# Performance work log

Hardware: AMD Instinct MI355X
Metric: run time of the kernel (lower is better)

## Reference

```python
import jax, jax.numpy as jnp
import numpy as np
import math

D_MODEL, N_HEAD, N_KV_HEAD, MAX_LEN = 2048, 32, 8, 2048
D_K = D_MODEL // N_HEAD
BASE = 10000.0
B, T = 2, 2048


def _rope_tables(seq_len):
    # matches torch Rotary: cos/sin of shape [seq_len, D_K], repeat_interleave(2) over freq dim
    inv_freq = 1.0 / (BASE ** (jnp.arange(0, D_K, 2, dtype=jnp.float32) / D_K))
    t = jnp.arange(seq_len, dtype=jnp.float32)[:, None] * inv_freq  # [T, D_K/2]
    cos = jnp.repeat(jnp.cos(t), 2, axis=-1)  # [T, D_K]
    sin = jnp.repeat(jnp.sin(t), 2, axis=-1)
    return cos, sin


def _rotate_half(x):
    # faithful to source: x1 = even lanes, x2 = odd lanes, concat([-x2, x1], -1)
    x1, x2 = x[..., ::2], x[..., 1::2]
    return jnp.concatenate([-x2, x1], axis=-1)


def _apply_rope(x, cos, sin):
    return x * cos + _rotate_half(x) * sin


def setup_inputs() -> dict:
    key = jax.random.key(0)
    ks = jax.random.split(key, 5)
    s = 1.0 / math.sqrt(D_MODEL)
    x = jax.random.normal(ks[0], (B, T, D_MODEL), dtype=jnp.float32)
    Wq = jax.random.normal(ks[1], (D_MODEL, N_HEAD * D_K), dtype=jnp.float32) * s
    Wk = jax.random.normal(ks[2], (D_MODEL, N_KV_HEAD * D_K), dtype=jnp.float32) * s
    Wv = jax.random.normal(ks[3], (D_MODEL, N_KV_HEAD * D_K), dtype=jnp.float32) * s
    Wo = jax.random.normal(ks[4], (N_HEAD * D_K, D_MODEL), dtype=jnp.float32) * s
    mask = jnp.tril(jnp.ones((T, T), dtype=bool))  # causal
    return {"x": x, "mask": mask, "Wq": Wq, "Wk": Wk, "Wv": Wv, "Wo": Wo}


def reference(x, mask, Wq, Wk, Wv, Wo):
    b, t, _ = x.shape
    g = N_HEAD // N_KV_HEAD
    q = (x @ Wq).reshape(b, t, N_HEAD, D_K).transpose(0, 2, 1, 3)      # [B,H,T,d]
    k = (x @ Wk).reshape(b, t, N_KV_HEAD, D_K).transpose(0, 2, 1, 3)   # [B,Hkv,T,d]
    v = (x @ Wv).reshape(b, t, N_KV_HEAD, D_K).transpose(0, 2, 1, 3)
    cos, sin = _rope_tables(t)
    q = _apply_rope(q, cos, sin)
    k = _apply_rope(k, cos, sin)  # rope before/after repeat is identical per-head
    # grouped attention: q head h attends kv head h // g (repeat_interleave semantics)
    qg = q.reshape(b, N_KV_HEAD, g, t, D_K)
    scores = jnp.einsum("bkgtd,bksd->bkgts", qg, k) / math.sqrt(D_K)
    neg = jnp.finfo(scores.dtype).min
    scores = jnp.where(mask[None, None, None, :, :], scores, neg)
    attn = jax.nn.softmax(scores, axis=-1)
    out = jnp.einsum("bkgts,bksd->bkgtd", attn, v)
    out = out.reshape(b, N_HEAD, t, D_K).transpose(0, 2, 1, 3).reshape(b, t, N_HEAD * D_K)
    return out @ Wo
```

## Files before the change

### kernel.cpp

```cpp
#include <hip/hip_runtime.h>
#include <cstdint>
#include <cstddef>

typedef unsigned short u16;
typedef __attribute__((ext_vector_type(8))) short bf16x8;
typedef __attribute__((ext_vector_type(8))) unsigned short u16x8;
typedef __attribute__((ext_vector_type(4))) unsigned short u16x4;
typedef __attribute__((ext_vector_type(4))) float f32x4;

__device__ __forceinline__ unsigned short f2bf(float f) {
    union { float f; uint32_t u; } c; c.f = f;
    uint32_t u = c.u + 0x7fffu + ((c.u >> 16) & 1u);
    return (unsigned short)(u >> 16);
}
__device__ __forceinline__ float bf2f(unsigned short h) {
    union { uint32_t u; float f; } c; c.u = ((uint32_t)h) << 16;
    return c.f;
}
__device__ __forceinline__ uint32_t cvtpk(float a, float b) {
    uint32_t r;
    asm("v_cvt_pk_bf16_f32 %0, %1, %2" : "=v"(r) : "v"(a), "v"(b));
    return r;
}

#define GLDS16(g, l)                                                               \
    __builtin_amdgcn_global_load_lds((const __attribute__((address_space(1))) void*)(g), \
                                     (__attribute__((address_space(3))) void*)(l), 16, 0, 0)

__global__ __launch_bounds__(256) void cvt_x(const float* __restrict__ src,
                                             u16* __restrict__ dst) {
    int i = blockIdx.x * 256 + threadIdx.x;
    const float4* s = (const float4*)src + (size_t)i * 2;
    float4 a = s[0], b = s[1];
    u16x8 o;
    o[0] = f2bf(a.x); o[1] = f2bf(a.y); o[2] = f2bf(a.z); o[3] = f2bf(a.w);
    o[4] = f2bf(b.x); o[5] = f2bf(b.y); o[6] = f2bf(b.z); o[7] = f2bf(b.w);
    *(u16x8*)(dst + (size_t)i * 8) = o;
}

__global__ __launch_bounds__(256) void tcvt(const float* __restrict__ src,
                                            u16* __restrict__ dst, int C) {
    __shared__ u16 tile[32][33];
    const int t = threadIdx.x;
    const int bx = blockIdx.x, by = blockIdx.y;
    const int tr = t >> 3, tc = (t & 7) << 2;
    float4 f = *(const float4*)&src[(size_t)(by * 32 + tr) * C + bx * 32 + tc];
    tile[tr][tc + 0] = f2bf(f.x); tile[tr][tc + 1] = f2bf(f.y);
    tile[tr][tc + 2] = f2bf(f.z); tile[tr][tc + 3] = f2bf(f.w);
    __syncthreads();
    u16x4 o;
    o[0] = tile[tc + 0][tr]; o[1] = tile[tc + 1][tr];
    o[2] = tile[tc + 2][tr]; o[3] = tile[tc + 3][tr];
    *(u16x4*)&dst[(size_t)(bx * 32 + tr) * 2048 + by * 32 + tc] = o;
}

__global__ __launch_bounds__(256) void tcvt3(const float* __restrict__ Wq,
                                             const float* __restrict__ Wk,
                                             const float* __restrict__ Wv,
                                             u16* __restrict__ dst) {
    __shared__ u16 tile[32][33];
    const int t = threadIdx.x;
    const int bxg = blockIdx.x, by = blockIdx.y;
    const float* src; int C, nb; u16* dbase;
    if (bxg < 64)      { src = Wq; C = 2048; nb = bxg;      dbase = dst; }
    else if (bxg < 80) { src = Wk; C = 512;  nb = bxg - 64; dbase = dst + (size_t)2048 * 2048; }
    else               { src = Wv; C = 512;  nb = bxg - 80; dbase = dst + (size_t)2560 * 2048; }
    const int tr = t >> 3, tc = (t & 7) << 2;
    float4 f = *(const float4*)&src[(size_t)(by * 32 + tr) * C + nb * 32 + tc];
    tile[tr][tc + 0] = f2bf(f.x); tile[tr][tc + 1] = f2bf(f.y);
    tile[tr][tc + 2] = f2bf(f.z); tile[tr][tc + 3] = f2bf(f.w);
    __syncthreads();
    u16x4 o;
    o[0] = tile[tc + 0][tr]; o[1] = tile[tc + 1][tr];
    o[2] = tile[tc + 2][tr]; o[3] = tile[tc + 3][tr];
    *(u16x4*)&dbase[(size_t)(nb * 32 + tr) * 2048 + by * 32 + tc] = o;
}

template <int MODE>
__global__ __launch_bounds__(256) void gemm2(const u16* __restrict__ A,
                                             const u16* __restrict__ Bt,
                                             u16* __restrict__ oq, u16* __restrict__ ok,
                                             u16* __restrict__ ov, float* __restrict__ of) {
    __shared__ u16 As[128 * 32];
    __shared__ u16 Bs[128 * 32];
    const int t = threadIdx.x, w = t >> 6, lane = t & 63;
    const int l15 = lane & 15, quad = lane >> 4;
    const int m0 = blockIdx.y << 7, n0 = blockIdx.x << 7;
    const int K = 2048;
    const int c0 = w * 2, c1 = c0 + 1;
    const int ar0 = c0 * 16 + (lane >> 2), ar1 = c1 * 16 + (lane >> 2);
    const int ac = (lane & 3) << 3;
    const u16* Ap0 = A + (size_t)(m0 + ar0) * K + ac;
    const u16* Ap1 = A + (size_t)(m0 + ar1) * K + ac;
    const u16* Bp0 = Bt + (size_t)(n0 + ar0) * K + ac;
    const u16* Bp1 = Bt + (size_t)(n0 + ar1) * K + ac;
    const int wm = (w >> 1) << 6, wn = (w & 1) << 6;

    f32x4 acc[4][4] = {};

    for (int k0 = 0; k0 < K; k0 += 32) {
        GLDS16(Ap0 + k0, &As[c0 * 512]);
        GLDS16(Ap1 + k0, &As[c1 * 512]);
        GLDS16(Bp0 + k0, &Bs[c0 * 512]);
        GLDS16(Bp1 + k0, &Bs[c1 * 512]);
        __syncthreads();
        bf16x8 a[4], bfr[4];
#pragma unroll
        for (int mt = 0; mt < 4; ++mt)
            a[mt] = *(bf16x8*)&As[(wm + mt * 16 + l15) * 32 + quad * 8];
#pragma unroll
        for (int nt = 0; nt < 4; ++nt)
            bfr[nt] = *(bf16x8*)&Bs[(wn + nt * 16 + l15) * 32 + quad * 8];
#pragma unroll
        for (int mt = 0; mt < 4; ++mt)
#pragma unroll
            for (int nt = 0; nt < 4; ++nt)
                acc[mt][nt] = __builtin_amdgcn_mfma_f32_16x16x32_bf16(a[mt], bfr[nt], acc[mt][nt], 0, 0, 0);
        __syncthreads();
    }

    if constexpr (MODE == 0) {
        const int colbase = n0 + wn;
        const bool isv = (colbase >= 2560);
        float iv[4];
        if (!isv) {
#pragma unroll
            for (int nt = 0; nt < 4; ++nt)
                iv[nt] = exp2f(-0.4152410118609253f * (float)(nt * 8 + (l15 >> 1)));
        }
        const int map1 = (quad << 4) | ((2 * l15 + 1) & 15);
        const int map2 = (quad << 4) | ((2 * l15) & 15);
        const bool lo = (l15 < 8);
#pragma unroll
        for (int mt = 0; mt < 4; ++mt)
#pragma unroll
            for (int r = 0; r < 4; ++r) {
                const int row = m0 + wm + mt * 16 + quad * 4 + r;
                float v0 = acc[mt][0][r], v1 = acc[mt][1][r];
                float v2 = acc[mt][2][r], v3 = acc[mt][3][r];
                float o0 = v0, o1 = v1, o2 = v2, o3 = v3;
                if (!isv) {
                    float g1a = __shfl(v0, map1), g1b = __shfl(v1, map1);
                    float g1c = __shfl(v2, map1), g1d = __shfl(v3, map1);
                    float g2a = __shfl(v0, map2), g2b = __shfl(v1, map2);
                    float g2c = __shfl(v2, map2), g2d = __shfl(v3, map2);
                    float p0 = lo ? g1a : g1b;
                    float p1 = lo ? g1c : g1d;
                    float p2 = lo ? g2a : g2b;
                    float p3 = lo ? g2c : g2d;
                    const float tt = (float)(row & 2047);
                    float sn, cs;
                    __sincosf(tt * iv[0], &sn, &cs); o0 = v0 * cs - p0 * sn;
                    __sincosf(tt * iv[1], &sn, &cs); o1 = v1 * cs - p1 * sn;
                    __sincosf(tt * iv[2], &sn, &cs); o2 = v2 * cs + p2 * sn;
                    __sincosf(tt * iv[3], &sn, &cs); o3 = v3 * cs + p3 * sn;
                }
                float o[4] = {o0, o1, o2, o3};
                if (colbase < 2048) {
#pragma unroll
                    for (int nt = 0; nt < 4; ++nt)
                        oq[(size_t)row * 2048 + colbase + nt * 16 + l15] = f2bf(o[nt]);
                } else if (colbase < 2560) {
#pragma unroll
                    for (int nt = 0; nt < 4; ++nt)
                        ok[(size_t)row * 512 + colbase - 2048 + nt * 16 + l15] = f2bf(o[nt]);
                } else {
#pragma unroll
                    for (int nt = 0; nt < 4; ++nt)
                        ov[(size_t)(colbase - 2560 + nt * 16 + l15) * 4096 + row] = f2bf(o[nt]);
                }
            }
    } else {
#pragma unroll
        for (int mt = 0; mt < 4; ++mt)
#pragma unroll
            for (int nt = 0; nt < 4; ++nt)
#pragma unroll
                for (int r = 0; r < 4; ++r) {
                    int row = m0 + wm + mt * 16 + quad * 4 + r;
                    int col = n0 + wn + nt * 16 + l15;
                    of[(size_t)row * 2048 + col] = acc[mt][nt][r];
                }
    }
}

__global__ __launch_bounds__(256, 2) void attn8(const u16* __restrict__ q,
                                                const u16* __restrict__ k,
                                                const u16* __restrict__ vT,
                                                u16* __restrict__ att) {
    __shared__ u16 Ks[64 * 64];
    __shared__ u16 Vt[64 * 64];
    __shared__ u16 Pw[4][2][16 * 64];

    const int t = threadIdx.x, w = t >> 6, lane = t & 63;
    const int l15 = lane & 15, quad = lane >> 4;
    const int id = blockIdx.x;
    const int kvh = id & 7;
    const int z = (id >> 3) & 1;
    const int gi = id >> 4;
    const int p = gi & 15;
    int g;
    switch (gi >> 4) {
        case 0:  g = 63 - p; break;
        case 1:  g = 32 + p; break;
        case 2:  g = 31 - p; break;
        default: g = p;      break;
    }
    const int h = kvh * 4 + w;
    const size_t rowbase = (size_t)z * 2048;
    const float SC = 0.125f * 1.4426950408889634f;
    const int swz = l15 & 7;

    const int srow = t >> 3;
    const int slot = t & 7;
    const int sd = slot << 3;
    const int lidx = srow * 64 + ((slot ^ (srow & 7)) << 3);

    const u16* kbase = &k[(rowbase + srow) * 512 + kvh * 64 + sd];
    const u16* vbase = &vT[(size_t)(kvh * 64 + srow) * 4096 + rowbase + sd];

    const int ntiles = (g >> 1) + 1;
    const int qrow0 = g * 32;

    bf16x8 aq[2][2];
#pragma unroll
    for (int m = 0; m < 2; ++m)
#pragma unroll
        for (int kc = 0; kc < 2; ++kc)
            aq[m][kc] = *(const bf16x8*)&q[(rowbase + qrow0 + m * 16 + l15) * 2048 +
                                           h * 64 + kc * 32 + quad * 8];

    f32x4 acc[2][4] = {};
    float m_i[2] = {-INFINITY, -INFINITY};
    float l_i[2] = {0.f, 0.f};

    u16x8 pk0 = *(const u16x8*)kbase;
    u16x8 pk1 = *(const u16x8*)(kbase + (size_t)32 * 512);
    u16x8 pv0 = *(const u16x8*)vbase;
    u16x8 pv1 = *(const u16x8*)(vbase + (size_t)32 * 4096);

    for (int kb = 0; kb < ntiles; ++kb) {
        __syncthreads();
        *(u16x8*)&Ks[lidx]        = pk0;
        *(u16x8*)&Ks[lidx + 2048] = pk1;
        *(u16x8*)&Vt[lidx]        = pv0;
        *(u16x8*)&Vt[lidx + 2048] = pv1;
        if (kb + 1 < ntiles) {
            const u16* kp = kbase + (size_t)(kb + 1) * 64 * 512;
            pk0 = *(const u16x8*)kp;
            pk1 = *(const u16x8*)(kp + (size_t)32 * 512);
            const u16* vp = vbase + (size_t)(kb + 1) * 64;
            pv0 = *(const u16x8*)vp;
            pv1 = *(const u16x8*)(vp + (size_t)32 * 4096);
        }
        __syncthreads();

        f32x4 st[2][4] = {};
        __builtin_amdgcn_s_setprio(1);
#pragma unroll
        for (int kt = 0; kt < 4; ++kt) {
            bf16x8 ak0 = *(const bf16x8*)&Ks[(kt * 16 + l15) * 64 + ((quad ^ swz) << 3)];
            bf16x8 ak1 = *(const bf16x8*)&Ks[(kt * 16 + l15) * 64 + (((quad + 4) ^ swz) << 3)];
#pragma unroll
            for (int m = 0; m < 2; ++m) {
                st[m][kt] = __builtin_amdgcn_mfma_f32_16x16x32_bf16(ak0, aq[m][0], st[m][kt], 0, 0, 0);
                st[m][kt] = __builtin_amdgcn_mfma_f32_16x16x32_bf16(ak1, aq[m][1], st[m][kt], 0, 0, 0);
            }
        }
        __builtin_amdgcn_s_setprio(0);

        const bool diag = (kb == ntiles - 1);
        float alpha_[2];
        bool resc[2];
#pragma unroll
        for (int m = 0; m < 2; ++m) {
            float sv[16];
#pragma unroll
            for (int kt = 0; kt < 4; ++kt)
#pragma unroll
                for (int r = 0; r < 4; ++r) sv[kt * 4 + r] = st[m][kt][r];
            if (diag) {
                const int qg = qrow0 + m * 16 + l15;
#pragma unroll
                for (int kt = 0; kt < 4; ++kt)
#pragma unroll
                    for (int r = 0; r < 4; ++r) {
                        int key = kb * 64 + kt * 16 + quad * 4 + r;
                        if (key > qg) sv[kt * 4 + r] = -INFINITY;
                    }
            }
            float mx = sv[0];
#pragma unroll
            for (int i = 1; i < 16; ++i) mx = fmaxf(mx, sv[i]);
            mx = fmaxf(mx, __shfl_xor(mx, 16));
            mx = fmaxf(mx, __shfl_xor(mx, 32));
            mx *= SC;
            const float mold = m_i[m];
            const bool need = __any(mx > mold + 8.f);
            float al = 1.f;
            if (need) {
                const float mnew = fmaxf(mold, mx);
                al = __builtin_amdgcn_exp2f(mold - mnew);
                m_i[m] = mnew;
            }
            const float mu = m_i[m];
            float sum = 0.f;
#pragma unroll
            for (int i = 0; i < 16; ++i) {
                sv[i] = __builtin_amdgcn_exp2f(fmaf(sv[i], SC, -mu));
                sum += sv[i];
            }
            sum += __shfl_xor(sum, 16);
            sum += __shfl_xor(sum, 32);
            l_i[m] = l_i[m] * al + sum;
            alpha_[m] = al;
            resc[m] = need;

            u16* Pq = &Pw[w][m][0];
#pragma unroll
            for (int kt = 0; kt < 4; ++kt) {
                uint2 uu;
                uu.x = cvtpk(sv[kt * 4 + 0], sv[kt * 4 + 1]);
                uu.y = cvtpk(sv[kt * 4 + 2], sv[kt * 4 + 3]);
                *(uint2*)&Pq[l15 * 64 + (((2 * kt + (quad >> 1)) ^ swz) << 3) + ((quad & 1) << 2)] = uu;
            }
        }

#pragma unroll
        for (int m = 0; m < 2; ++m)
            if (resc[m]) {
                const float al = alpha_[m];
#pragma unroll
                for (int dt = 0; dt < 4; ++dt)
#pragma unroll
                    for (int r = 0; r < 4; ++r) acc[m][dt][r] *= al;
            }

        bf16x8 bp[2][2];
#pragma unroll
        for (int m = 0; m < 2; ++m) {
            const u16* Pq = &Pw[w][m][0];
            bp[m][0] = *(const bf16x8*)&Pq[l15 * 64 + ((quad ^ swz) << 3)];
            bp[m][1] = *(const bf16x8*)&Pq[l15 * 64 + (((quad + 4) ^ swz) << 3)];
        }

        __builtin_amdgcn_s_setprio(1);
#pragma unroll
        for (int dt = 0; dt < 4; ++dt) {
            bf16x8 av0 = *(const bf16x8*)&Vt[(dt * 16 + l15) * 64 + ((quad ^ swz) << 3)];
            bf16x8 av1 = *(const bf16x8*)&Vt[(dt * 16 + l15) * 64 + (((quad + 4) ^ swz) << 3)];
#pragma unroll
            for (int m = 0; m < 2; ++m) {
                acc[m][dt] = __builtin_amdgcn_mfma_f32_16x16x32_bf16(av0, bp[m][0], acc[m][dt], 0, 0, 0);
                acc[m][dt] = __builtin_amdgcn_mfma_f32_16x16x32_bf16(av1, bp[m][1], acc[m][dt], 0, 0, 0);
            }
        }
        __builtin_amdgcn_s_setprio(0);
    }

#pragma unroll
    for (int m = 0; m < 2; ++m) {
        float inv = 1.0f / l_i[m];
        size_t row = rowbase + qrow0 + m * 16 + l15;
#pragma unroll
        for (int dt = 0; dt < 4; ++dt) {
            uint2 uu;
            uu.x = cvtpk(acc[m][dt][0] * inv, acc[m][dt][1] * inv);
            uu.y = cvtpk(acc[m][dt][2] * inv, acc[m][dt][3] * inv);
            *(uint2*)&att[row * 2048 + h * 64 + dt * 16 + quad * 4] = uu;
        }
    }
}

extern "C" void kernel_launch(void* const* d_in, const int* in_sizes, int n_in,
                              void* d_out, int out_size, void* d_ws, size_t ws_size,
                              hipStream_t stream) {
    const float* x  = (const float*)d_in[0];
    const float* Wq = (const float*)d_in[2];
    const float* Wk = (const float*)d_in[3];
    const float* Wv = (const float*)d_in[4];
    const float* Wo = (const float*)d_in[5];
    float* out = (float*)d_out;

    u16* xb = (u16*)d_out;

    u16* q     = (u16*)d_ws;
    u16* kk    = q + (size_t)4096 * 2048;
    u16* vt    = kk + (size_t)4096 * 512;
    u16* wqkvt = vt + (size_t)4096 * 512;
    u16* att   = wqkvt;
    u16* wot   = kk;

    cvt_x<<<4096, 256, 0, stream>>>(x, xb);
    tcvt3<<<dim3(96, 64), 256, 0, stream>>>(Wq, Wk, Wv, wqkvt);
    gemm2<0><<<dim3(24, 32), 256, 0, stream>>>(xb, wqkvt, q, kk, vt, nullptr);
    attn8<<<1024, 256, 0, stream>>>(q, kk, vt, att);
    tcvt<<<dim3(64, 64), 256, 0, stream>>>(Wo, wot, 2048);
    gemm2<1><<<dim3(16, 32), 256, 0, stream>>>(att, wot, nullptr, nullptr, nullptr, out);
}
```

Before: 311.6 us.

## Replace QKV projection GEMM with 256x256 tile, 8-wave ping-pong pipelined kernel

```diff
diff --git a/kernel.cpp b/kernel.cpp
--- a/kernel.cpp
+++ b/kernel.cpp
@@ -119,69 +119,183 @@
         __syncthreads();
     }
 
-    if constexpr (MODE == 0) {
-        const int colbase = n0 + wn;
-        const bool isv = (colbase >= 2560);
-        float iv[4];
-        if (!isv) {
-#pragma unroll
-            for (int nt = 0; nt < 4; ++nt)
-                iv[nt] = exp2f(-0.4152410118609253f * (float)(nt * 8 + (l15 >> 1)));
-        }
-        const int map1 = (quad << 4) | ((2 * l15 + 1) & 15);
-        const int map2 = (quad << 4) | ((2 * l15) & 15);
-        const bool lo = (l15 < 8);
-#pragma unroll
-        for (int mt = 0; mt < 4; ++mt)
+#pragma unroll
+    for (int mt = 0; mt < 4; ++mt)
+#pragma unroll
+        for (int nt = 0; nt < 4; ++nt)
 #pragma unroll
             for (int r = 0; r < 4; ++r) {
-                const int row = m0 + wm + mt * 16 + quad * 4 + r;
-                float v0 = acc[mt][0][r], v1 = acc[mt][1][r];
-                float v2 = acc[mt][2][r], v3 = acc[mt][3][r];
-                float o0 = v0, o1 = v1, o2 = v2, o3 = v3;
-                if (!isv) {
-                    float g1a = __shfl(v0, map1), g1b = __shfl(v1, map1);
-                    float g1c = __shfl(v2, map1), g1d = __shfl(v3, map1);
-                    float g2a = __shfl(v0, map2), g2b = __shfl(v1, map2);
-                    float g2c = __shfl(v2, map2), g2d = __shfl(v3, map2);
-                    float p0 = lo ? g1a : g1b;
-                    float p1 = lo ? g1c : g1d;
-                    float p2 = lo ? g2a : g2b;
-                    float p3 = lo ? g2c : g2d;
-                    const float tt = (float)(row & 2047);
-                    float sn, cs;
-                    __sincosf(tt * iv[0], &sn, &cs); o0 = v0 * cs - p0 * sn;
-                    __sincosf(tt * iv[1], &sn, &cs); o1 = v1 * cs - p1 * sn;
-                    __sincosf(tt * iv[2], &sn, &cs); o2 = v2 * cs + p2 * sn;
-                    __sincosf(tt * iv[3], &sn, &cs); o3 = v3 * cs + p3 * sn;
-                }
-                float o[4] = {o0, o1, o2, o3};
-                if (colbase < 2048) {
-#pragma unroll
-                    for (int nt = 0; nt < 4; ++nt)
-                        oq[(size_t)row * 2048 + colbase + nt * 16 + l15] = f2bf(o[nt]);
-                } else if (colbase < 2560) {
-#pragma unroll
-                    for (int nt = 0; nt < 4; ++nt)
-                        ok[(size_t)row * 512 + colbase - 2048 + nt * 16 + l15] = f2bf(o[nt]);
-                } else {
-#pragma unroll
-                    for (int nt = 0; nt < 4; ++nt)
-                        ov[(size_t)(colbase - 2560 + nt * 16 + l15) * 4096 + row] = f2bf(o[nt]);
-                }
-            }
-    } else {
-#pragma unroll
-        for (int mt = 0; mt < 4; ++mt)
-#pragma unroll
-            for (int nt = 0; nt < 4; ++nt)
-#pragma unroll
-                for (int r = 0; r < 4; ++r) {
-                    int row = m0 + wm + mt * 16 + quad * 4 + r;
-                    int col = n0 + wn + nt * 16 + l15;
-                    of[(size_t)row * 2048 + col] = acc[mt][nt][r];
-                }
-    }
+                int row = m0 + wm + mt * 16 + quad * 4 + r;
+                int col = n0 + wn + nt * 16 + l15;
+                of[(size_t)row * 2048 + col] = acc[mt][nt][r];
+            }
+}
+
+__global__ __launch_bounds__(512, 1) void gemm8p(const u16* __restrict__ A,
+                                                 const u16* __restrict__ Bt,
+                                                 u16* __restrict__ oq, u16* __restrict__ ok,
+                                                 u16* __restrict__ ov) {
+    __shared__ u16 lds[65536];
+
+    const int t = threadIdx.x, w = t >> 6, lane = t & 63;
+    const int l15 = lane & 15, quad = lane >> 4;
+    const int wm = w >> 2, wn = w & 3;
+    const int m0 = blockIdx.y << 8, n0 = blockIdx.x << 8;
+    const int K = 2048;
+    const int NIT = 16;
+
+    const int srow = w * 8 + (lane >> 3);
+    const int scol = ((lane & 7) ^ (lane >> 3)) << 3;
+    const u16* pA = A + (size_t)(m0 + srow) * K + scol;
+    const u16* pB = Bt + (size_t)(n0 + srow) * K + scol;
+
+#define STG(AB, BUF, HF, T) do {                                                   \
+    const u16* _s = ((AB) ? pB : pA) + (size_t)((HF) * 128) * K + (size_t)(T) * 64; \
+    u16* _d = &lds[(BUF) * 32768 + (AB) * 16384 + (HF) * 8192 + w * 512];          \
+    GLDS16(_s, _d);                                                                \
+    GLDS16(_s + (size_t)64 * K, _d + 4096);                                        \
+} while (0)
+
+#define RD_A(BUF, MQ)                                                              \
+    _Pragma("unroll") for (int fi = 0; fi < 4; ++fi)                               \
+    _Pragma("unroll") for (int ks = 0; ks < 2; ++ks) {                             \
+        int r_ = (MQ) * 64 + fi * 16 + l15;                                        \
+        int u_ = ks * 4 + quad;                                                    \
+        a_[fi][ks] = *(const bf16x8*)&lds[(BUF) * 32768 + wm * 8192 + r_ * 64 +    \
+                                          ((u_ ^ (r_ & 7)) << 3)];                 \
+    }
+#define RD_B(BUF, NQ)                                                              \
+    _Pragma("unroll") for (int fj = 0; fj < 2; ++fj)                               \
+    _Pragma("unroll") for (int ks = 0; ks < 2; ++ks) {                             \
+        int r_ = (wn & 1) * 64 + (NQ) * 32 + fj * 16 + l15;                        \
+        int u_ = ks * 4 + quad;                                                    \
+        b_[fj][ks] = *(const bf16x8*)&lds[(BUF) * 32768 + 16384 + (wn >> 1) * 8192 \
+                                          + r_ * 64 + ((u_ ^ (r_ & 7)) << 3)];     \
+    }
+#define MFMA16(MQ, NQ)                                                             \
+    __builtin_amdgcn_s_barrier();                                                  \
+    asm volatile("s_waitcnt lgkmcnt(0)" ::: "memory");                             \
+    __builtin_amdgcn_sched_barrier(0);                                             \
+    __builtin_amdgcn_s_setprio(1);                                                 \
+    _Pragma("unroll") for (int fi = 0; fi < 4; ++fi)                               \
+    _Pragma("unroll") for (int fj = 0; fj < 2; ++fj) {                             \
+        acc[(MQ) * 4 + fi][(NQ) * 2 + fj] = __builtin_amdgcn_mfma_f32_16x16x32_bf16( \
+            a_[fi][0], b_[fj][0], acc[(MQ) * 4 + fi][(NQ) * 2 + fj], 0, 0, 0);     \
+        acc[(MQ) * 4 + fi][(NQ) * 2 + fj] = __builtin_amdgcn_mfma_f32_16x16x32_bf16( \
+            a_[fi][1], b_[fj][1], acc[(MQ) * 4 + fi][(NQ) * 2 + fj], 0, 0, 0);     \
+    }                                                                              \
+    __builtin_amdgcn_s_setprio(0);
+
+    f32x4 acc[8][4] = {};
+    bf16x8 a_[4][2], b_[2][2];
+
+    STG(0, 0, 0, 0); STG(0, 0, 1, 0);
+    STG(1, 0, 0, 0); STG(1, 0, 1, 0);
+    STG(1, 1, 0, 1); STG(1, 1, 1, 1);
+    asm volatile("s_waitcnt vmcnt(4)" ::: "memory");
+    __builtin_amdgcn_s_barrier();
+
+    for (int it = 0; it < NIT; ++it) {
+        const bool more = (it + 1 < NIT);
+        const int o = 2 * it + 1, e2 = 2 * it + 2, o2 = 2 * it + 3;
+
+        RD_A(0, 0); RD_B(0, 0);
+        STG(0, 1, 0, o);
+        MFMA16(0, 0);
+        __builtin_amdgcn_s_barrier();
+
+        RD_A(0, 1);
+        STG(0, 1, 1, o);
+        MFMA16(1, 0);
+        __builtin_amdgcn_s_barrier();
+
+        RD_A(0, 0); RD_B(0, 1);
+        MFMA16(0, 1);
+        __builtin_amdgcn_s_barrier();
+
+        RD_A(0, 1);
+        if (more) { STG(1, 0, 0, e2); STG(1, 0, 1, e2); }
+        MFMA16(1, 1);
+        if (more) asm volatile("s_waitcnt vmcnt(4)" ::: "memory");
+        else      asm volatile("s_waitcnt vmcnt(0)" ::: "memory");
+        __builtin_amdgcn_s_barrier();
+
+        RD_A(1, 0); RD_B(1, 0);
+        if (more) STG(0, 0, 0, e2);
+        MFMA16(0, 0);
+        __builtin_amdgcn_s_barrier();
+
+        RD_A(1, 1);
+        if (more) STG(0, 0, 1, e2);
+        MFMA16(1, 0);
+        __builtin_amdgcn_s_barrier();
+
+        RD_A(1, 0); RD_B(1, 1);
+        MFMA16(0, 1);
+        __builtin_amdgcn_s_barrier();
+
+        RD_A(1, 1);
+        if (more) { STG(1, 1, 0, o2); STG(1, 1, 1, o2); }
+        MFMA16(1, 1);
+        if (more) asm volatile("s_waitcnt vmcnt(4)" ::: "memory");
+        else      asm volatile("s_waitcnt vmcnt(0)" ::: "memory");
+        __builtin_amdgcn_s_barrier();
+    }
+#undef STG
+#undef RD_A
+#undef RD_B
+#undef MFMA16
+
+    const int colbase = n0 + wn * 64;
+    const bool isv = (colbase >= 2560);
+    float iv[4];
+    if (!isv) {
+#pragma unroll
+        for (int nj = 0; nj < 4; ++nj)
+            iv[nj] = exp2f(-0.4152410118609253f * (float)(nj * 8 + (l15 >> 1)));
+    }
+    const int map1 = (quad << 4) | ((2 * l15 + 1) & 15);
+    const int map2 = (quad << 4) | ((2 * l15) & 15);
+    const bool lo = (l15 < 8);
+#pragma unroll
+    for (int mi = 0; mi < 8; ++mi)
+#pragma unroll
+        for (int r = 0; r < 4; ++r) {
+            const int row = m0 + wm * 128 + mi * 16 + quad * 4 + r;
+            float v0 = acc[mi][0][r], v1 = acc[mi][1][r];
+            float v2 = acc[mi][2][r], v3 = acc[mi][3][r];
+            float o0 = v0, o1 = v1, o2 = v2, o3 = v3;
+            if (!isv) {
+                float g1a = __shfl(v0, map1), g1b = __shfl(v1, map1);
+                float g1c = __shfl(v2, map1), g1d = __shfl(v3, map1);
+                float g2a = __shfl(v0, map2), g2b = __shfl(v1, map2);
+                float g2c = __shfl(v2, map2), g2d = __shfl(v3, map2);
+                float p0 = lo ? g1a : g1b;
+                float p1 = lo ? g1c : g1d;
+                float p2 = lo ? g2a : g2b;
+                float p3 = lo ? g2c : g2d;
+                const float tt = (float)(row & 2047);
+                float sn, cs;
+                __sincosf(tt * iv[0], &sn, &cs); o0 = v0 * cs - p0 * sn;
+                __sincosf(tt * iv[1], &sn, &cs); o1 = v1 * cs - p1 * sn;
+                __sincosf(tt * iv[2], &sn, &cs); o2 = v2 * cs + p2 * sn;
+                __sincosf(tt * iv[3], &sn, &cs); o3 = v3 * cs + p3 * sn;
+            }
+            float oo[4] = {o0, o1, o2, o3};
+            if (colbase < 2048) {
+#pragma unroll
+                for (int nj = 0; nj < 4; ++nj)
+                    oq[(size_t)row * 2048 + colbase + nj * 16 + l15] = f2bf(oo[nj]);
+            } else if (colbase < 2560) {
+#pragma unroll
+                for (int nj = 0; nj < 4; ++nj)
+                    ok[(size_t)row * 512 + colbase - 2048 + nj * 16 + l15] = f2bf(oo[nj]);
+            } else {
+#pragma unroll
+                for (int nj = 0; nj < 4; ++nj)
+                    ov[(size_t)(colbase - 2560 + nj * 16 + l15) * 4096 + row] = f2bf(oo[nj]);
+            }
+        }
 }
 
 __global__ __launch_bounds__(256, 2) void attn8(const u16* __restrict__ q,
@@ -393,7 +507,7 @@
 
     cvt_x<<<4096, 256, 0, stream>>>(x, xb);
     tcvt3<<<dim3(96, 64), 256, 0, stream>>>(Wq, Wk, Wv, wqkvt);
-    gemm2<0><<<dim3(24, 32), 256, 0, stream>>>(xb, wqkvt, q, kk, vt, nullptr);
+    gemm8p<<<dim3(12, 16), 512, 0, stream>>>(xb, wqkvt, q, kk, vt);
     attn8<<<1024, 256, 0, stream>>>(q, kk, vt, att);
     tcvt<<<dim3(64, 64), 256, 0, stream>>>(Wo, wot, 2048);
     gemm2<1><<<dim3(16, 32), 256, 0, stream>>>(att, wot, nullptr, nullptr, nullptr, out);
```

Result: slower. 330.7 us (+6.1%).

## Double-buffer K/V tiles in attention and fuse all conversion kernels into one launch

Applied to the files above, without the earlier changes.

```diff
diff --git a/kernel.cpp b/kernel.cpp
--- a/kernel.cpp
+++ b/kernel.cpp
@@ -27,15 +27,49 @@
     __builtin_amdgcn_global_load_lds((const __attribute__((address_space(1))) void*)(g), \
                                      (__attribute__((address_space(3))) void*)(l), 16, 0, 0)
 
-__global__ __launch_bounds__(256) void cvt_x(const float* __restrict__ src,
-                                             u16* __restrict__ dst) {
-    int i = blockIdx.x * 256 + threadIdx.x;
-    const float4* s = (const float4*)src + (size_t)i * 2;
-    float4 a = s[0], b = s[1];
-    u16x8 o;
-    o[0] = f2bf(a.x); o[1] = f2bf(a.y); o[2] = f2bf(a.z); o[3] = f2bf(a.w);
-    o[4] = f2bf(b.x); o[5] = f2bf(b.y); o[6] = f2bf(b.z); o[7] = f2bf(b.w);
-    *(u16x8*)(dst + (size_t)i * 8) = o;
+__global__ __launch_bounds__(256) void prep(const float* __restrict__ x,
+                                            const float* __restrict__ Wq,
+                                            const float* __restrict__ Wk,
+                                            const float* __restrict__ Wv,
+                                            const float* __restrict__ Wo,
+                                            u16* __restrict__ xb,
+                                            u16* __restrict__ wqkvt,
+                                            u16* __restrict__ wot) {
+    __shared__ u16 tile[32][33];
+    const int id = blockIdx.x;
+    const int t = threadIdx.x;
+
+    if (id < 4096) {
+        int i = id * 256 + t;
+        const float4* s = (const float4*)x + (size_t)i * 2;
+        float4 a = s[0], b = s[1];
+        u16x8 o;
+        o[0] = f2bf(a.x); o[1] = f2bf(a.y); o[2] = f2bf(a.z); o[3] = f2bf(a.w);
+        o[4] = f2bf(b.x); o[5] = f2bf(b.y); o[6] = f2bf(b.z); o[7] = f2bf(b.w);
+        *(u16x8*)(xb + (size_t)i * 8) = o;
+        return;
+    }
+
+    const float* src; int C, nb, by; u16* dbase;
+    if (id < 10240) {
+        int r = id - 4096;
+        int bxg = r % 96; by = r / 96;
+        if (bxg < 64)      { src = Wq; C = 2048; nb = bxg;      dbase = wqkvt; }
+        else if (bxg < 80) { src = Wk; C = 512;  nb = bxg - 64; dbase = wqkvt + (size_t)2048 * 2048; }
+        else               { src = Wv; C = 512;  nb = bxg - 80; dbase = wqkvt + (size_t)2560 * 2048; }
+    } else {
+        int r = id - 10240;
+        nb = r % 64; by = r / 64; src = Wo; C = 2048; dbase = wot;
+    }
+    const int tr = t >> 3, tc = (t & 7) << 2;
+    float4 f = *(const float4*)&src[(size_t)(by * 32 + tr) * C + nb * 32 + tc];
+    tile[tr][tc + 0] = f2bf(f.x); tile[tr][tc + 1] = f2bf(f.y);
+    tile[tr][tc + 2] = f2bf(f.z); tile[tr][tc + 3] = f2bf(f.w);
+    __syncthreads();
+    u16x4 o;
+    o[0] = tile[tc + 0][tr]; o[1] = tile[tc + 1][tr];
+    o[2] = tile[tc + 2][tr]; o[3] = tile[tc + 3][tr];
+    *(u16x4*)&dbase[(size_t)(nb * 32 + tr) * 2048 + by * 32 + tc] = o;
 }
 
 __global__ __launch_bounds__(256) void tcvt(const float* __restrict__ src,
@@ -52,28 +86,6 @@
     o[0] = tile[tc + 0][tr]; o[1] = tile[tc + 1][tr];
     o[2] = tile[tc + 2][tr]; o[3] = tile[tc + 3][tr];
     *(u16x4*)&dst[(size_t)(bx * 32 + tr) * 2048 + by * 32 + tc] = o;
-}
-
-__global__ __launch_bounds__(256) void tcvt3(const float* __restrict__ Wq,
-                                             const float* __restrict__ Wk,
-                                             const float* __restrict__ Wv,
-                                             u16* __restrict__ dst) {
-    __shared__ u16 tile[32][33];
-    const int t = threadIdx.x;
-    const int bxg = blockIdx.x, by = blockIdx.y;
-    const float* src; int C, nb; u16* dbase;
-    if (bxg < 64)      { src = Wq; C = 2048; nb = bxg;      dbase = dst; }
-    else if (bxg < 80) { src = Wk; C = 512;  nb = bxg - 64; dbase = dst + (size_t)2048 * 2048; }
-    else               { src = Wv; C = 512;  nb = bxg - 80; dbase = dst + (size_t)2560 * 2048; }
-    const int tr = t >> 3, tc = (t & 7) << 2;
-    float4 f = *(const float4*)&src[(size_t)(by * 32 + tr) * C + nb * 32 + tc];
-    tile[tr][tc + 0] = f2bf(f.x); tile[tr][tc + 1] = f2bf(f.y);
-    tile[tr][tc + 2] = f2bf(f.z); tile[tr][tc + 3] = f2bf(f.w);
-    __syncthreads();
-    u16x4 o;
-    o[0] = tile[tc + 0][tr]; o[1] = tile[tc + 1][tr];
-    o[2] = tile[tc + 2][tr]; o[3] = tile[tc + 3][tr];
-    *(u16x4*)&dbase[(size_t)(nb * 32 + tr) * 2048 + by * 32 + tc] = o;
 }
 
 template <int MODE>
@@ -184,12 +196,12 @@
     }
 }
 
-__global__ __launch_bounds__(256, 2) void attn8(const u16* __restrict__ q,
-                                                const u16* __restrict__ k,
-                                                const u16* __restrict__ vT,
-                                                u16* __restrict__ att) {
-    __shared__ u16 Ks[64 * 64];
-    __shared__ u16 Vt[64 * 64];
+__global__ __launch_bounds__(256, 2) void attn10(const u16* __restrict__ q,
+                                                 const u16* __restrict__ k,
+                                                 const u16* __restrict__ vT,
+                                                 u16* __restrict__ att) {
+    __shared__ u16 Ks[2][64 * 64];
+    __shared__ u16 Vt[2][64 * 64];
     __shared__ u16 Pw[4][2][16 * 64];
 
     const int t = threadIdx.x, w = t >> 6, lane = t & 63;
@@ -238,29 +250,29 @@
     u16x8 pk1 = *(const u16x8*)(kbase + (size_t)32 * 512);
     u16x8 pv0 = *(const u16x8*)vbase;
     u16x8 pv1 = *(const u16x8*)(vbase + (size_t)32 * 4096);
+    *(u16x8*)&Ks[0][lidx]        = pk0;
+    *(u16x8*)&Ks[0][lidx + 2048] = pk1;
+    *(u16x8*)&Vt[0][lidx]        = pv0;
+    *(u16x8*)&Vt[0][lidx + 2048] = pv1;
+    if (ntiles > 1) {
+        const u16* kp = kbase + (size_t)64 * 512;
+        pk0 = *(const u16x8*)kp;
+        pk1 = *(const u16x8*)(kp + (size_t)32 * 512);
+        const u16* vp = vbase + 64;
+        pv0 = *(const u16x8*)vp;
+        pv1 = *(const u16x8*)(vp + (size_t)32 * 4096);
+    }
+    __syncthreads();
 
     for (int kb = 0; kb < ntiles; ++kb) {
-        __syncthreads();
-        *(u16x8*)&Ks[lidx]        = pk0;
-        *(u16x8*)&Ks[lidx + 2048] = pk1;
-        *(u16x8*)&Vt[lidx]        = pv0;
-        *(u16x8*)&Vt[lidx + 2048] = pv1;
-        if (kb + 1 < ntiles) {
-            const u16* kp = kbase + (size_t)(kb + 1) * 64 * 512;
-            pk0 = *(const u16x8*)kp;
-            pk1 = *(const u16x8*)(kp + (size_t)32 * 512);
-            const u16* vp = vbase + (size_t)(kb + 1) * 64;
-            pv0 = *(const u16x8*)vp;
-            pv1 = *(const u16x8*)(vp + (size_t)32 * 4096);
-        }
-        __syncthreads();
+        const int cur = kb & 1;
 
         f32x4 st[2][4] = {};
         __builtin_amdgcn_s_setprio(1);
 #pragma unroll
         for (int kt = 0; kt < 4; ++kt) {
-            bf16x8 ak0 = *(const bf16x8*)&Ks[(kt * 16 + l15) * 64 + ((quad ^ swz) << 3)];
-            bf16x8 ak1 = *(const bf16x8*)&Ks[(kt * 16 + l15) * 64 + (((quad + 4) ^ swz) << 3)];
+            bf16x8 ak0 = *(const bf16x8*)&Ks[cur][(kt * 16 + l15) * 64 + ((quad ^ swz) << 3)];
+            bf16x8 ak1 = *(const bf16x8*)&Ks[cur][(kt * 16 + l15) * 64 + (((quad + 4) ^ swz) << 3)];
 #pragma unroll
             for (int m = 0; m < 2; ++m) {
                 st[m][kt] = __builtin_amdgcn_mfma_f32_16x16x32_bf16(ak0, aq[m][0], st[m][kt], 0, 0, 0);
@@ -326,6 +338,22 @@
             }
         }
 
+        if (kb + 1 < ntiles) {
+            const int nx = cur ^ 1;
+            *(u16x8*)&Ks[nx][lidx]        = pk0;
+            *(u16x8*)&Ks[nx][lidx + 2048] = pk1;
+            *(u16x8*)&Vt[nx][lidx]        = pv0;
+            *(u16x8*)&Vt[nx][lidx + 2048] = pv1;
+            if (kb + 2 < ntiles) {
+                const u16* kp = kbase + (size_t)(kb + 2) * 64 * 512;
+                pk0 = *(const u16x8*)kp;
+                pk1 = *(const u16x8*)(kp + (size_t)32 * 512);
+                const u16* vp = vbase + (size_t)(kb + 2) * 64;
+                pv0 = *(const u16x8*)vp;
+                pv1 = *(const u16x8*)(vp + (size_t)32 * 4096);
+            }
+        }
+
 #pragma unroll
         for (int m = 0; m < 2; ++m)
             if (resc[m]) {
@@ -347,8 +375,8 @@
         __builtin_amdgcn_s_setprio(1);
 #pragma unroll
         for (int dt = 0; dt < 4; ++dt) {
-            bf16x8 av0 = *(const bf16x8*)&Vt[(dt * 16 + l15) * 64 + ((quad ^ swz) << 3)];
-            bf16x8 av1 = *(const bf16x8*)&Vt[(dt * 16 + l15) * 64 + (((quad + 4) ^ swz) << 3)];
+            bf16x8 av0 = *(const bf16x8*)&Vt[cur][(dt * 16 + l15) * 64 + ((quad ^ swz) << 3)];
+            bf16x8 av1 = *(const bf16x8*)&Vt[cur][(dt * 16 + l15) * 64 + (((quad + 4) ^ swz) << 3)];
 #pragma unroll
             for (int m = 0; m < 2; ++m) {
                 acc[m][dt] = __builtin_amdgcn_mfma_f32_16x16x32_bf16(av0, bp[m][0], acc[m][dt], 0, 0, 0);
@@ -356,6 +384,7 @@
             }
         }
         __builtin_amdgcn_s_setprio(0);
+        __syncthreads();
     }
 
 #pragma unroll
@@ -389,12 +418,22 @@
     u16* vt    = kk + (size_t)4096 * 512;
     u16* wqkvt = vt + (size_t)4096 * 512;
     u16* att   = wqkvt;
-    u16* wot   = kk;
-
-    cvt_x<<<4096, 256, 0, stream>>>(x, xb);
-    tcvt3<<<dim3(96, 64), 256, 0, stream>>>(Wq, Wk, Wv, wqkvt);
-    gemm2<0><<<dim3(24, 32), 256, 0, stream>>>(xb, wqkvt, q, kk, vt, nullptr);
-    attn8<<<1024, 256, 0, stream>>>(q, kk, vt, att);
-    tcvt<<<dim3(64, 64), 256, 0, stream>>>(Wo, wot, 2048);
-    gemm2<1><<<dim3(16, 32), 256, 0, stream>>>(att, wot, nullptr, nullptr, nullptr, out);
-}
+    u16* wot_sep = att + (size_t)4096 * 2048;
+
+    const size_t need = ((size_t)4096 * 2048 + 4096 * 512 + 512 * 4096 +
+                         (size_t)4096 * 2048 + (size_t)2048 * 2048) * 2;
+
+    if (ws_size >= need) {
+        prep<<<14336, 256, 0, stream>>>(x, Wq, Wk, Wv, Wo, xb, wqkvt, wot_sep);
+        gemm2<0><<<dim3(24, 32), 256, 0, stream>>>(xb, wqkvt, q, kk, vt, nullptr);
+        attn10<<<1024, 256, 0, stream>>>(q, kk, vt, att);
+        gemm2<1><<<dim3(16, 32), 256, 0, stream>>>(att, wot_sep, nullptr, nullptr, nullptr, out);
+    } else {
+        u16* wot = kk;
+        prep<<<10240, 256, 0, stream>>>(x, Wq, Wk, Wv, Wo, xb, wqkvt, nullptr);
+        gemm2<0><<<dim3(24, 32), 256, 0, stream>>>(xb, wqkvt, q, kk, vt, nullptr);
+        attn10<<<1024, 256, 0, stream>>>(q, kk, vt, att);
+        tcvt<<<dim3(64, 64), 256, 0, stream>>>(Wo, wot, 2048);
+        gemm2<1><<<dim3(16, 32), 256, 0, stream>>>(att, wot, nullptr, nullptr, nullptr, out);
+    }
+}
```

New measurement: 301.4 us. 3.3% less time.
